# Kernel optimization log

Measured on AMD Instinct MI355X. Metric: run time of the kernel, lower is better.

## Reference

```python
import jax, jax.numpy as jnp
import numpy as np

NEG_SLOPE = 0.01  # F.leaky_relu default used in the original forward


def setup_inputs() -> dict:
    key = jax.random.key(0)
    ks = jax.random.split(key, 6)
    B, N, D = 2, 4096, 128
    s = 1.0 / np.sqrt(D)
    return {
        "embed_feat": jax.random.normal(ks[0], (B, N, D), jnp.float32),
        "predict_G": 1,
        "W_demand": jax.random.normal(ks[1], (D,), jnp.float32) * s,
        "b_demand": jnp.zeros((1,), jnp.float32),
        "Wa": jax.random.normal(ks[2], (D, D), jnp.float32) * s,
        "w_l": jax.random.normal(ks[3], (D,), jnp.float32) * s,
        "w_r": jax.random.normal(ks[4], (D,), jnp.float32) * s,
    }


def reference(embed_feat, predict_G, W_demand, b_demand, Wa, w_l, w_r):
    # demands: sigmoid(Linear(D->1)) -> [B, N]
    demands = jax.nn.sigmoid(embed_feat @ W_demand + b_demand[0])
    if not predict_G:
        return (demands, None)
    # proj = Wa(x): [B, N, D]  (torch Linear: x @ Wa.T)
    proj = jnp.einsum('bnd,ed->bne', embed_feat, Wa)
    # per-node scalar scores; A[b,i,j] = l[b,i] + r[b,j] (vectorized form of the O(N^2) loop)
    l = proj @ w_l  # [B, N]
    r = proj @ w_r  # [B, N]
    A = jax.nn.leaky_relu(l[:, :, None] + r[:, None, :], negative_slope=NEG_SLOPE)
    # original softmax over dim=1 of [N, N, 1] == over j axis
    Q = jax.nn.softmax(A, axis=2)  # [B, N, N]
    # rel_Ds[b,i,j] = demands[b,i]
    Gs = Q * demands[:, :, None]
    return (demands, Gs)
```

## Files before the change

kernel.cpp:

```cpp
#include <hip/hip_runtime.h>
#include <stdint.h>

#define N 4096
#define B 2
#define D 128
#define LOG2E 1.4426950408889634f

typedef float f32x4 __attribute__((ext_vector_type(4)));

__device__ __forceinline__ float lrelu(float t) { return t > 0.f ? t : 0.01f * t; }

__global__ __launch_bounds__(256) void k1_uvec(
    const float* __restrict__ Wa,
    const float* __restrict__ w_l,
    const float* __restrict__ w_r,
    float* __restrict__ u) {
    __shared__ float2 pl[4][64];
    __shared__ float2 pr[4][64];
    int t = threadIdx.x;
    int d2 = t & 63;
    int h = t >> 6;
    const float2* Wa2 = (const float2*)Wa;
    float2 al = make_float2(0.f, 0.f), ar = make_float2(0.f, 0.f);
    #pragma unroll 8
    for (int k = 0; k < 32; ++k) {
        int e = h * 32 + k;
        float2 w = Wa2[e * 64 + d2];
        float wl = w_l[e];
        float wr = w_r[e];
        al.x += w.x * wl; al.y += w.y * wl;
        ar.x += w.x * wr; ar.y += w.y * wr;
    }
    pl[h][d2] = al; pr[h][d2] = ar;
    __syncthreads();
    if (t < 64) {
        float2 s = make_float2(0.f, 0.f);
        #pragma unroll
        for (int hh = 0; hh < 4; ++hh) { s.x += pl[hh][t].x; s.y += pl[hh][t].y; }
        ((float2*)u)[t] = s;
    } else if (t < 128) {
        int dd = t - 64;
        float2 s = make_float2(0.f, 0.f);
        #pragma unroll
        for (int hh = 0; hh < 4; ++hh) { s.x += pr[hh][dd].x; s.y += pr[hh][dd].y; }
        ((float2*)(u + D))[dd] = s;
    }
}

__global__ __launch_bounds__(256) void k2_rows(
    const float* __restrict__ x,
    const float* __restrict__ Wd,
    const float* __restrict__ bd,
    const float* __restrict__ u,
    float* __restrict__ out_dem,
    float* __restrict__ lv,
    float4* __restrict__ q4) {
    int lane = threadIdx.x & 63;
    int row = blockIdx.x * 4 + (threadIdx.x >> 6);
    float2 xv = ((const float2*)(x + (size_t)row * D))[lane];
    float2 ul2 = ((const float2*)u)[lane];
    float2 ur2 = ((const float2*)(u + D))[lane];
    float2 wv = ((const float2*)Wd)[lane];
    float pl = xv.x * ul2.x + xv.y * ul2.y;
    float pr = xv.x * ur2.x + xv.y * ur2.y;
    float pd = xv.x * wv.x + xv.y * wv.y;
    #pragma unroll
    for (int m = 32; m >= 1; m >>= 1) {
        pl += __shfl_xor(pl, m, 64);
        pr += __shfl_xor(pr, m, 64);
        pd += __shfl_xor(pd, m, 64);
    }
    if (lane == 0) {
        float dem = 1.f / (1.f + __expf(-(pd + bd[0])));
        out_dem[row] = dem;
        lv[row] = pl * LOG2E;
        q4[row].x = pr * LOG2E;
    }
}

__global__ __launch_bounds__(1024) void k2b_fpm(
    float4* __restrict__ q4,
    float* __restrict__ gmax) {
    __shared__ float red[16];
    int b = blockIdx.x;
    int tid = threadIdx.x;
    float4* qb = q4 + (size_t)b * N;
    float r[4];
    float m = -3.402823466e38f;
    #pragma unroll
    for (int k = 0; k < 4; ++k) {
        r[k] = qb[tid + k * 1024].x;
        m = fmaxf(m, r[k]);
    }
    #pragma unroll
    for (int s = 32; s >= 1; s >>= 1) m = fmaxf(m, __shfl_xor(m, s, 64));
    if ((tid & 63) == 0) red[tid >> 6] = m;
    __syncthreads();
    float rmax = red[0];
    #pragma unroll
    for (int w = 1; w < 16; ++w) rmax = fmaxf(rmax, red[w]);
    if (tid == 0) gmax[b] = rmax;
    #pragma unroll
    for (int k = 0; k < 4; ++k) {
        float t = r[k] - rmax;
        qb[tid + k * 1024] = make_float4(r[k], exp2f(t), exp2f(0.01f * t), 0.f);
    }
}

__global__ __launch_bounds__(256) void k3_main(
    const float* __restrict__ lv,
    const float4* __restrict__ q4,
    const float* __restrict__ gmax,
    const float* __restrict__ dem_f,
    float* __restrict__ out_g) {
    __shared__ float red[4][8];
    int tid = threadIdx.x;
    int b = blockIdx.x >> 10;
    int i0 = (blockIdx.x & 1023) << 2;
    const float4* qb = q4 + (size_t)b * N;
    float rmax = gmax[b];
    int rowbase = b * N + i0;

    float l_[4];
    #pragma unroll
    for (int q = 0; q < 4; ++q) l_[q] = lv[rowbase + q];

    float s1[4] = {0.f, 0.f, 0.f, 0.f}, s2[4] = {0.f, 0.f, 0.f, 0.f};
    #pragma unroll 4
    for (int k = 0; k < N / 256; ++k) {
        float4 v = qb[tid + k * 256];
        #pragma unroll
        for (int q = 0; q < 4; ++q) {
            bool pos = (l_[q] + v.x) > 0.f;
            s1[q] += pos ? v.y : 0.f;
            s2[q] += pos ? 0.f : v.z;
        }
    }
    #pragma unroll
    for (int m = 32; m >= 1; m >>= 1) {
        #pragma unroll
        for (int q = 0; q < 4; ++q) {
            s1[q] += __shfl_xor(s1[q], m, 64);
            s2[q] += __shfl_xor(s2[q], m, 64);
        }
    }
    int w = tid >> 6;
    if ((tid & 63) == 0) {
        #pragma unroll
        for (int q = 0; q < 4; ++q) { red[w][q] = s1[q]; red[w][4 + q] = s2[q]; }
    }
    __syncthreads();
    float eP[4], eM[4];
    #pragma unroll
    for (int q = 0; q < 4; ++q) {
        float S1 = red[0][q] + red[1][q] + red[2][q] + red[3][q];
        float S2 = red[0][4 + q] + red[1][4 + q] + red[2][4 + q] + red[3][4 + q];
        float t0 = l_[q] + rmax;
        float m0 = lrelu(t0);
        float Ep = exp2f(t0 - m0);
        float Em = exp2f(0.01f * t0 - m0);
        float sc = dem_f[rowbase + q] / (Ep * S1 + Em * S2);
        eP[q] = Ep * sc;
        eM[q] = Em * sc;
    }

    size_t gbase = (size_t)b * N * N + (size_t)i0 * N;
    #pragma unroll
    for (int it = 0; it < 4; ++it) {
        int idx = it * 256 + tid;
        float4 v0 = qb[idx * 4 + 0];
        float4 v1 = qb[idx * 4 + 1];
        float4 v2 = qb[idx * 4 + 2];
        float4 v3 = qb[idx * 4 + 3];
        #pragma unroll
        for (int q = 0; q < 4; ++q) {
            f32x4 o;
            o.x = (l_[q] + v0.x > 0.f) ? eP[q] * v0.y : eM[q] * v0.z;
            o.y = (l_[q] + v1.x > 0.f) ? eP[q] * v1.y : eM[q] * v1.z;
            o.z = (l_[q] + v2.x > 0.f) ? eP[q] * v2.y : eM[q] * v2.z;
            o.w = (l_[q] + v3.x > 0.f) ? eP[q] * v3.y : eM[q] * v3.z;
            *((f32x4*)(out_g + gbase + (size_t)q * N) + idx) = o;
        }
    }
}

extern "C" void kernel_launch(void* const* d_in, const int* in_sizes, int n_in,
                              void* d_out, int out_size, void* d_ws, size_t ws_size,
                              hipStream_t stream) {
    const float* x  = (const float*)d_in[0];
    const float* Wd = (const float*)d_in[2];
    const float* bd = (const float*)d_in[3];
    const float* Wa = (const float*)d_in[4];
    const float* wl = (const float*)d_in[5];
    const float* wr = (const float*)d_in[6];

    float* ws = (float*)d_ws;
    float* u  = ws;
    float* lv = ws + 256;
    float4* q4 = (float4*)(ws + 256 + 8192);
    float* gmax = ws + 256 + 8192 + 4 * 8192;

    float* out     = (float*)d_out;
    float* out_dem = out;
    float* out_g   = out + B * N;

    hipLaunchKernelGGL(k1_uvec, dim3(1), dim3(256), 0, stream, Wa, wl, wr, u);
    hipLaunchKernelGGL(k2_rows, dim3(B * N / 4), dim3(256), 0, stream,
                       x, Wd, bd, u, out_dem, lv, q4);
    hipLaunchKernelGGL(k2b_fpm, dim3(B), dim3(1024), 0, stream, q4, gmax);
    hipLaunchKernelGGL(k3_main, dim3(B * N / 4), dim3(256), 0, stream,
                       lv, q4, gmax, out_dem, out_g);
}
```

Measured before the change: 160.6 us.

## Split fused softmax kernel into denominator pass and flat streaming write kernel

Column data moves from an interleaved float4 array to three separate planar arrays (r, exp-pos, exp-neg), so the denominator reduction reads vectorized float4 chunks. The former fused kernel becomes two: one computes per-row scale factors into a rowfac buffer, the other streams the full N×N output with a flat grid-stride index where each thread reads row factors and column vectors. The aim is a simpler, fully coalesced output write with more parallelism, at the cost of an extra launch and extra global reads of row and column factors per output element.

```diff
diff --git a/kernel.cpp b/kernel.cpp
--- a/kernel.cpp
+++ b/kernel.cpp
@@ -54,7 +54,7 @@
     const float* __restrict__ u,
     float* __restrict__ out_dem,
     float* __restrict__ lv,
-    float4* __restrict__ q4) {
+    float* __restrict__ colR) {
     int lane = threadIdx.x & 63;
     int row = blockIdx.x * 4 + (threadIdx.x >> 6);
     float2 xv = ((const float2*)(x + (size_t)row * D))[lane];
@@ -74,22 +74,24 @@
         float dem = 1.f / (1.f + __expf(-(pd + bd[0])));
         out_dem[row] = dem;
         lv[row] = pl * LOG2E;
-        q4[row].x = pr * LOG2E;
+        colR[row] = pr * LOG2E;
     }
 }
 
 __global__ __launch_bounds__(1024) void k2b_fpm(
-    float4* __restrict__ q4,
+    const float* __restrict__ colR,
+    float* __restrict__ colFp,
+    float* __restrict__ colFm,
     float* __restrict__ gmax) {
     __shared__ float red[16];
     int b = blockIdx.x;
     int tid = threadIdx.x;
-    float4* qb = q4 + (size_t)b * N;
+    const float* rb = colR + (size_t)b * N;
     float r[4];
     float m = -3.402823466e38f;
     #pragma unroll
     for (int k = 0; k < 4; ++k) {
-        r[k] = qb[tid + k * 1024].x;
+        r[k] = rb[tid + k * 1024];
         m = fmaxf(m, r[k]);
     }
     #pragma unroll
@@ -103,21 +105,26 @@
     #pragma unroll
     for (int k = 0; k < 4; ++k) {
         float t = r[k] - rmax;
-        qb[tid + k * 1024] = make_float4(r[k], exp2f(t), exp2f(0.01f * t), 0.f);
-    }
-}
-
-__global__ __launch_bounds__(256) void k3_main(
+        colFp[(size_t)b * N + tid + k * 1024] = exp2f(t);
+        colFm[(size_t)b * N + tid + k * 1024] = exp2f(0.01f * t);
+    }
+}
+
+__global__ __launch_bounds__(256) void k2c_den(
     const float* __restrict__ lv,
-    const float4* __restrict__ q4,
+    const float* __restrict__ colR,
+    const float* __restrict__ colFp,
+    const float* __restrict__ colFm,
     const float* __restrict__ gmax,
     const float* __restrict__ dem_f,
-    float* __restrict__ out_g) {
+    float4* __restrict__ rowfac) {
     __shared__ float red[4][8];
     int tid = threadIdx.x;
     int b = blockIdx.x >> 10;
     int i0 = (blockIdx.x & 1023) << 2;
-    const float4* qb = q4 + (size_t)b * N;
+    const float4* r4 = (const float4*)(colR + (size_t)b * N);
+    const float4* p4 = (const float4*)(colFp + (size_t)b * N);
+    const float4* m4 = (const float4*)(colFm + (size_t)b * N);
     float rmax = gmax[b];
     int rowbase = b * N + i0;
 
@@ -127,13 +134,21 @@
 
     float s1[4] = {0.f, 0.f, 0.f, 0.f}, s2[4] = {0.f, 0.f, 0.f, 0.f};
     #pragma unroll 4
-    for (int k = 0; k < N / 256; ++k) {
-        float4 v = qb[tid + k * 256];
+    for (int k = 0; k < N / 4 / 256; ++k) {
+        float4 rv = r4[tid + k * 256];
+        float4 fp = p4[tid + k * 256];
+        float4 fm = m4[tid + k * 256];
         #pragma unroll
         for (int q = 0; q < 4; ++q) {
-            bool pos = (l_[q] + v.x) > 0.f;
-            s1[q] += pos ? v.y : 0.f;
-            s2[q] += pos ? 0.f : v.z;
+            float l = l_[q];
+            s1[q] += (l + rv.x > 0.f) ? fp.x : 0.f;
+            s2[q] += (l + rv.x > 0.f) ? 0.f : fm.x;
+            s1[q] += (l + rv.y > 0.f) ? fp.y : 0.f;
+            s2[q] += (l + rv.y > 0.f) ? 0.f : fm.y;
+            s1[q] += (l + rv.z > 0.f) ? fp.z : 0.f;
+            s2[q] += (l + rv.z > 0.f) ? 0.f : fm.z;
+            s1[q] += (l + rv.w > 0.f) ? fp.w : 0.f;
+            s2[q] += (l + rv.w > 0.f) ? 0.f : fm.w;
         }
     }
     #pragma unroll
@@ -150,9 +165,8 @@
         for (int q = 0; q < 4; ++q) { red[w][q] = s1[q]; red[w][4 + q] = s2[q]; }
     }
     __syncthreads();
-    float eP[4], eM[4];
-    #pragma unroll
-    for (int q = 0; q < 4; ++q) {
+    if (tid < 4) {
+        int q = tid;
         float S1 = red[0][q] + red[1][q] + red[2][q] + red[3][q];
         float S2 = red[0][4 + q] + red[1][4 + q] + red[2][4 + q] + red[3][4 + q];
         float t0 = l_[q] + rmax;
@@ -160,27 +174,35 @@
         float Ep = exp2f(t0 - m0);
         float Em = exp2f(0.01f * t0 - m0);
         float sc = dem_f[rowbase + q] / (Ep * S1 + Em * S2);
-        eP[q] = Ep * sc;
-        eM[q] = Em * sc;
-    }
-
-    size_t gbase = (size_t)b * N * N + (size_t)i0 * N;
+        rowfac[rowbase + q] = make_float4(l_[q], Ep * sc, Em * sc, 0.f);
+    }
+}
+
+__global__ __launch_bounds__(256) void k3w_write(
+    const float4* __restrict__ rowfac,
+    const float* __restrict__ colR,
+    const float* __restrict__ colFp,
+    const float* __restrict__ colFm,
+    float* __restrict__ out_g) {
+    const int STRIDE = 8192 * 256;
+    int g0 = blockIdx.x * 256 + threadIdx.x;
     #pragma unroll
     for (int it = 0; it < 4; ++it) {
-        int idx = it * 256 + tid;
-        float4 v0 = qb[idx * 4 + 0];
-        float4 v1 = qb[idx * 4 + 1];
-        float4 v2 = qb[idx * 4 + 2];
-        float4 v3 = qb[idx * 4 + 3];
-        #pragma unroll
-        for (int q = 0; q < 4; ++q) {
-            f32x4 o;
-            o.x = (l_[q] + v0.x > 0.f) ? eP[q] * v0.y : eM[q] * v0.z;
-            o.y = (l_[q] + v1.x > 0.f) ? eP[q] * v1.y : eM[q] * v1.z;
-            o.z = (l_[q] + v2.x > 0.f) ? eP[q] * v2.y : eM[q] * v2.z;
-            o.w = (l_[q] + v3.x > 0.f) ? eP[q] * v3.y : eM[q] * v3.z;
-            *((f32x4*)(out_g + gbase + (size_t)q * N) + idx) = o;
-        }
+        int g = g0 + it * STRIDE;
+        int j4 = g & 1023;
+        int i  = (g >> 10) & 4095;
+        int bb = g >> 22;
+        float4 rf = rowfac[(bb << 12) + i];
+        int cb = (bb << 12) + (j4 << 2);
+        float4 rv = *(const float4*)(colR + cb);
+        float4 fp = *(const float4*)(colFp + cb);
+        float4 fm = *(const float4*)(colFm + cb);
+        f32x4 o;
+        o.x = (rf.x + rv.x > 0.f) ? rf.y * fp.x : rf.z * fm.x;
+        o.y = (rf.x + rv.y > 0.f) ? rf.y * fp.y : rf.z * fm.y;
+        o.z = (rf.x + rv.z > 0.f) ? rf.y * fp.z : rf.z * fm.z;
+        o.w = (rf.x + rv.w > 0.f) ? rf.y * fp.w : rf.z * fm.w;
+        *((f32x4*)out_g + g) = o;
     }
 }
 
@@ -195,10 +217,13 @@
     const float* wr = (const float*)d_in[6];
 
     float* ws = (float*)d_ws;
-    float* u  = ws;
-    float* lv = ws + 256;
-    float4* q4 = (float4*)(ws + 256 + 8192);
-    float* gmax = ws + 256 + 8192 + 4 * 8192;
+    float* u      = ws;
+    float* lv     = ws + 256;
+    float* colR   = ws + 256 + 8192;
+    float* colFp  = colR + 8192;
+    float* colFm  = colFp + 8192;
+    float4* rowfac = (float4*)(colFm + 8192);
+    float* gmax   = (float*)(rowfac + 8192);
 
     float* out     = (float*)d_out;
     float* out_dem = out;
@@ -206,8 +231,11 @@
 
     hipLaunchKernelGGL(k1_uvec, dim3(1), dim3(256), 0, stream, Wa, wl, wr, u);
     hipLaunchKernelGGL(k2_rows, dim3(B * N / 4), dim3(256), 0, stream,
-                       x, Wd, bd, u, out_dem, lv, q4);
-    hipLaunchKernelGGL(k2b_fpm, dim3(B), dim3(1024), 0, stream, q4, gmax);
-    hipLaunchKernelGGL(k3_main, dim3(B * N / 4), dim3(256), 0, stream,
-                       lv, q4, gmax, out_dem, out_g);
-}
+                       x, Wd, bd, u, out_dem, lv, colR);
+    hipLaunchKernelGGL(k2b_fpm, dim3(B), dim3(1024), 0, stream,
+                       colR, colFp, colFm, gmax);
+    hipLaunchKernelGGL(k2c_den, dim3(B * N / 4), dim3(256), 0, stream,
+                       lv, colR, colFp, colFm, gmax, out_dem, rowfac);
+    hipLaunchKernelGGL(k3w_write, dim3(8192), dim3(256), 0, stream,
+                       rowfac, colR, colFp, colFm, out_g);
+}
```

Measured after the change: 172.3 us. 1.07x slower.
